# Kernel tuning notes

Measured on AMD Instinct MI355X. Metric: run time of the kernel, lower is better.

The kernel has to match this reference:

```python
import jax, jax.numpy as jnp
import numpy as np

T, N = 64, 128          # temporal / spatial graph sizes; M = T*N product-graph nodes
B, F_IN, HID, F_OUT = 2, 32, 32, 16
L, K = 2, 4             # num_layers, filter order


def _sym_norm(key, n):
    # random symmetric adjacency, then D^{-1/2} A D^{-1/2} / 2 as in the torch __init__
    a = jax.random.uniform(key, (n, n), dtype=jnp.float32)
    a = 0.5 * (a + a.T)
    d = jnp.sum(a, axis=1)
    dinv = 1.0 / jnp.sqrt(d)
    return (dinv[:, None] * a * dinv[None, :]) * 0.5


def setup_inputs() -> dict:
    key = jax.random.key(0)
    ks = jax.random.split(key, 9)
    x = jax.random.normal(ks[0], (B, T * N, F_IN), dtype=jnp.float32)
    Adj_t = _sym_norm(ks[1], T)
    Adj_s = _sym_norm(ks[2], N)
    s = jax.random.normal(ks[3], (4,), dtype=jnp.float32) * 0.25
    H = jax.random.normal(ks[4], (L, K, HID, HID), dtype=jnp.float32) * 0.1
    W1 = jax.random.normal(ks[5], (F_IN, HID), dtype=jnp.float32) * (1.0 / np.sqrt(F_IN))
    b1 = jax.random.normal(ks[6], (HID,), dtype=jnp.float32) * 0.01
    W2 = jax.random.normal(ks[7], (HID, F_OUT), dtype=jnp.float32) * (1.0 / np.sqrt(HID))
    b2 = jax.random.normal(ks[8], (F_OUT,), dtype=jnp.float32) * 0.01
    return {"x": x, "Adj_t": Adj_t, "Adj_s": Adj_s, "s": s, "H": H,
            "W1": W1, "b1": b1, "W2": W2, "b2": b2}


def reference(x, Adj_t, Adj_s, s, H, W1, b1, W2, b2):
    t, n = Adj_t.shape[0], Adj_s.shape[0]
    I_t = jnp.eye(t, dtype=jnp.float32)
    I_s = jnp.eye(n, dtype=jnp.float32)
    # Adj = s0*I + s1*kron(I_t, Adj_s) + s2*kron(Adj_t, I_s) + s3*kron(Adj_t, Adj_s)
    Adj = (s[0] * jnp.eye(t * n, dtype=jnp.float32)
           + s[1] * jnp.kron(I_t, Adj_s)
           + s[2] * jnp.kron(Adj_t, I_s)
           + s[3] * jnp.kron(Adj_t, Adj_s))
    h = x @ W1 + b1                                   # [B, M, HID]
    num_layers = H.shape[0]
    for l in range(num_layers):
        Ah = jnp.einsum('mn,bnh->bmh', Adj, h)        # Adj @ x, hoisted out of k-loop
        # sum_k (Adj@x) @ H[l,k]  ==  einsum over k and h simultaneously
        h = jnp.tanh(jnp.einsum('bmh,khf->bmf', Ah, H[l]))
    return h @ W2 + b2                                # [B, M, F_OUT]
```

## Files before the change

kernel.cpp:

```cpp
#include <hip/hip_runtime.h>


__device__ __forceinline__ int swz(int row, int g) { return g ^ (row & 7); }

template<bool PROJ>
__global__ __launch_bounds__(512) void k_temporal(
    const float* __restrict__ src,
    const float* __restrict__ At,
    const float* __restrict__ W1, const float* __restrict__ b1,
    const float* __restrict__ s,
    float* __restrict__ up, float* __restrict__ pp)
{
    __shared__ float At_s[64 * 64];
    __shared__ float xs  [64 * 32];
    __shared__ float hls [64 * 32];
    __shared__ float W1s [1024];

    const int tid = threadIdx.x;
    const int b   = blockIdx.x >> 7;
    const int n   = blockIdx.x & 127;
    const int fg  = tid >> 6;
    const int lt  = tid & 63;

    const float s0v = s[0], s1v = s[1], s2v = s[2], s3v = s[3];

#pragma unroll
    for (int i = 0; i < 8; ++i) {
        int p = tid + 512 * i;
        int r = p >> 6, c = p & 63;
        At_s[r * 64 + (swz(r, c >> 2) << 2) + (c & 3)] = At[p];
    }

    if (PROJ) {
        {
            int tt = tid >> 3, c4 = tid & 7;
            float4 v = *(const float4*)(src + ((size_t)(b * 8192 + tt * 128 + n)) * 32 + c4 * 4);
            *(float4*)&xs[tt * 32 + (swz(tt, c4) << 2)] = v;
        }
        if (tid < 256) ((float4*)W1s)[tid] = ((const float4*)W1)[tid];
        __syncthreads();
        float4 bv = *(const float4*)(b1 + fg * 4);
        float h0 = bv.x, h1 = bv.y, h2 = bv.z, h3 = bv.w;
#pragma unroll
        for (int k4 = 0; k4 < 8; ++k4) {
            float4 xv = *(const float4*)&xs[lt * 32 + (swz(lt, k4) << 2)];
            float4 w0 = *(const float4*)&W1s[(k4 * 4 + 0) * 32 + fg * 4];
            float4 w1 = *(const float4*)&W1s[(k4 * 4 + 1) * 32 + fg * 4];
            float4 w2 = *(const float4*)&W1s[(k4 * 4 + 2) * 32 + fg * 4];
            float4 w3 = *(const float4*)&W1s[(k4 * 4 + 3) * 32 + fg * 4];
            h0 += xv.x * w0.x + xv.y * w1.x + xv.z * w2.x + xv.w * w3.x;
            h1 += xv.x * w0.y + xv.y * w1.y + xv.z * w2.y + xv.w * w3.y;
            h2 += xv.x * w0.z + xv.y * w1.z + xv.z * w2.z + xv.w * w3.z;
            h3 += xv.x * w0.w + xv.y * w1.w + xv.z * w2.w + xv.w * w3.w;
        }
        float4 hv; hv.x = h0; hv.y = h1; hv.z = h2; hv.w = h3;
        *(float4*)&hls[lt * 32 + (swz(lt, fg) << 2)] = hv;
        __syncthreads();
    } else {
        {
            int tt = tid >> 3, c4 = tid & 7;
            float4 v = *(const float4*)(src + ((size_t)(b * 128 + n)) * 2048 + tt * 32 + c4 * 4);
            *(float4*)&hls[tt * 32 + (swz(tt, c4) << 2)] = v;
        }
        __syncthreads();
    }

    float4 hv = *(const float4*)&hls[lt * 32 + (swz(lt, fg) << 2)];
    float w0 = 0.f, w1 = 0.f, w2 = 0.f, w3 = 0.f;
#pragma unroll
    for (int u4 = 0; u4 < 16; ++u4) {
        float4 av = *(const float4*)&At_s[lt * 64 + (swz(lt, u4) << 2)];
        float4 g0 = *(const float4*)&hls[(u4 * 4 + 0) * 32 + (swz(u4 * 4 + 0, fg) << 2)];
        float4 g1 = *(const float4*)&hls[(u4 * 4 + 1) * 32 + (swz(u4 * 4 + 1, fg) << 2)];
        float4 g2 = *(const float4*)&hls[(u4 * 4 + 2) * 32 + (swz(u4 * 4 + 2, fg) << 2)];
        float4 g3 = *(const float4*)&hls[(u4 * 4 + 3) * 32 + (swz(u4 * 4 + 3, fg) << 2)];
        w0 += av.x * g0.x + av.y * g1.x + av.z * g2.x + av.w * g3.x;
        w1 += av.x * g0.y + av.y * g1.y + av.z * g2.y + av.w * g3.y;
        w2 += av.x * g0.z + av.y * g1.z + av.z * g2.z + av.w * g3.z;
        w3 += av.x * g0.w + av.y * g1.w + av.z * g2.w + av.w * g3.w;
    }
    float4 uo, po;
    uo.x = s1v * hv.x + s3v * w0;  po.x = s0v * hv.x + s2v * w0;
    uo.y = s1v * hv.y + s3v * w1;  po.y = s0v * hv.y + s2v * w1;
    uo.z = s1v * hv.z + s3v * w2;  po.z = s0v * hv.z + s2v * w2;
    uo.w = s1v * hv.w + s3v * w3;  po.w = s0v * hv.w + s2v * w3;
    size_t base = ((size_t)((b * 64 + lt) * 128 + n)) * 32 + fg * 4;
    *(float4*)(up + base) = uo;
    *(float4*)(pp + base) = po;
}

template<bool LAST>
__global__ __launch_bounds__(512) void k_spatial(
    const float* __restrict__ up, const float* __restrict__ pp,
    const float* __restrict__ As, const float* __restrict__ H, int layer,
    const float* __restrict__ W2, const float* __restrict__ b2,
    float* __restrict__ hout, float* __restrict__ out)
{
    __shared__ float As_s[64 * 128];
    __shared__ float up_s[128 * 32];
    __shared__ float Ah_s[64 * 32];
    __shared__ float T_s [64 * 32];
    __shared__ float Hs  [1024];
    __shared__ float W2s [512];

    const int tid = threadIdx.x;
    const int b   = blockIdx.x >> 7;
    const int t   = (blockIdx.x >> 1) & 63;
    const int mh  = blockIdx.x & 1;
    const int fg  = tid >> 6;
    const int m   = tid & 63;

#pragma unroll
    for (int i = 0; i < 4; ++i) {
        int p = tid + 512 * i;
        int r = p >> 5, g = p & 31;
        float4 v = *(const float4*)(As + ((size_t)(mh * 64 + r)) * 128 + g * 4);
        *(float4*)&As_s[r * 128 + (swz(r, g) << 2)] = v;
    }
    {
        const float* usrc = up + ((size_t)(b * 64 + t)) * 4096;
        ((float4*)up_s)[tid]       = ((const float4*)usrc)[tid];
        ((float4*)up_s)[tid + 512] = ((const float4*)usrc)[tid + 512];
    }
    {
        const float* Hl = H + layer * 4096;
#pragma unroll
        for (int i = 0; i < 2; ++i) {
            int p = tid + 512 * i;
            Hs[p] = Hl[p] + Hl[1024 + p] + Hl[2048 + p] + Hl[3072 + p];
        }
    }
    if (LAST && tid < 128) ((float4*)W2s)[tid] = ((const float4*)W2)[tid];
    float4 pv = *(const float4*)(pp + ((size_t)((b * 64 + t) * 128 + mh * 64 + m)) * 32 + fg * 4);
    float a0 = pv.x, a1 = pv.y, a2 = pv.z, a3 = pv.w;
    __syncthreads();

#pragma unroll 8
    for (int n4 = 0; n4 < 32; ++n4) {
        float4 av = *(const float4*)&As_s[m * 128 + (swz(m, n4) << 2)];
        float4 u0 = *(const float4*)&up_s[(n4 * 4 + 0) * 32 + fg * 4];
        float4 u1 = *(const float4*)&up_s[(n4 * 4 + 1) * 32 + fg * 4];
        float4 u2 = *(const float4*)&up_s[(n4 * 4 + 2) * 32 + fg * 4];
        float4 u3 = *(const float4*)&up_s[(n4 * 4 + 3) * 32 + fg * 4];
        a0 += av.x * u0.x + av.y * u1.x + av.z * u2.x + av.w * u3.x;
        a1 += av.x * u0.y + av.y * u1.y + av.z * u2.y + av.w * u3.y;
        a2 += av.x * u0.z + av.y * u1.z + av.z * u2.z + av.w * u3.z;
        a3 += av.x * u0.w + av.y * u1.w + av.z * u2.w + av.w * u3.w;
    }
    {
        float4 t4; t4.x = a0; t4.y = a1; t4.z = a2; t4.w = a3;
        *(float4*)&Ah_s[m * 32 + (swz(m, fg) << 2)] = t4;
    }
    __syncthreads();

    float c0 = 0.f, c1 = 0.f, c2 = 0.f, c3 = 0.f;
#pragma unroll
    for (int k4 = 0; k4 < 8; ++k4) {
        float4 av = *(const float4*)&Ah_s[m * 32 + (swz(m, k4) << 2)];
        float4 q0 = *(const float4*)&Hs[(k4 * 4 + 0) * 32 + fg * 4];
        float4 q1 = *(const float4*)&Hs[(k4 * 4 + 1) * 32 + fg * 4];
        float4 q2 = *(const float4*)&Hs[(k4 * 4 + 2) * 32 + fg * 4];
        float4 q3 = *(const float4*)&Hs[(k4 * 4 + 3) * 32 + fg * 4];
        c0 += av.x * q0.x + av.y * q1.x + av.z * q2.x + av.w * q3.x;
        c1 += av.x * q0.y + av.y * q1.y + av.z * q2.y + av.w * q3.y;
        c2 += av.x * q0.z + av.y * q1.z + av.z * q2.z + av.w * q3.z;
        c3 += av.x * q0.w + av.y * q1.w + av.z * q2.w + av.w * q3.w;
    }
    c0 = tanhf(c0); c1 = tanhf(c1); c2 = tanhf(c2); c3 = tanhf(c3);

    if (!LAST) {
        float4 o; o.x = c0; o.y = c1; o.z = c2; o.w = c3;
        *(float4*)(hout + (((size_t)(b * 128 + mh * 64 + m)) * 64 + t) * 32 + fg * 4) = o;
    } else {
        float4 t4; t4.x = c0; t4.y = c1; t4.z = c2; t4.w = c3;
        *(float4*)&T_s[m * 32 + (swz(m, fg) << 2)] = t4;
        __syncthreads();
        const int fo = fg * 2;
        float o0 = b2[fo], o1 = b2[fo + 1];
#pragma unroll
        for (int k4 = 0; k4 < 8; ++k4) {
            float4 tv = *(const float4*)&T_s[m * 32 + (swz(m, k4) << 2)];
            float2 v0 = *(const float2*)&W2s[(k4 * 4 + 0) * 16 + fo];
            float2 v1 = *(const float2*)&W2s[(k4 * 4 + 1) * 16 + fo];
            float2 v2 = *(const float2*)&W2s[(k4 * 4 + 2) * 16 + fo];
            float2 v3 = *(const float2*)&W2s[(k4 * 4 + 3) * 16 + fo];
            o0 += tv.x * v0.x + tv.y * v1.x + tv.z * v2.x + tv.w * v3.x;
            o1 += tv.x * v0.y + tv.y * v1.y + tv.z * v2.y + tv.w * v3.y;
        }
        float2 o2; o2.x = o0; o2.y = o1;
        *(float2*)(out + ((size_t)((b * 64 + t) * 128 + mh * 64 + m)) * 16 + fo) = o2;
    }
}

extern "C" void kernel_launch(void* const* d_in, const int* in_sizes, int n_in,
                              void* d_out, int out_size, void* d_ws, size_t ws_size,
                              hipStream_t stream)
{
    const float* x   = (const float*)d_in[0];
    const float* At  = (const float*)d_in[1];
    const float* As  = (const float*)d_in[2];
    const float* s   = (const float*)d_in[3];
    const float* H   = (const float*)d_in[4];
    const float* W1  = (const float*)d_in[5];
    const float* b1  = (const float*)d_in[6];
    const float* W2  = (const float*)d_in[7];
    const float* b2  = (const float*)d_in[8];
    float* out = (float*)d_out;

    float* up   = (float*)d_ws;
    float* pp   = up + 524288;
    float* hbuf = pp + 524288;

    k_temporal<true ><<<256, 512, 0, stream>>>(x,    At, W1, b1, s, up, pp);
    k_spatial <false><<<256, 512, 0, stream>>>(up, pp, As, H, 0, W2, b2, hbuf, out);
    k_temporal<false><<<256, 512, 0, stream>>>(hbuf, At, W1, b1, s, up, pp);
    k_spatial <true ><<<256, 512, 0, stream>>>(up, pp, As, H, 1, W2, b2, hbuf, out);
}
```

Baseline: 32.77 us.

## Broadcast matrix operands via wave readlane instead of shared-memory staging

Weight matrices (W1, summed H, W2) and intermediate activations (h, up rows) are kept distributed in registers across the 64 lanes of a wave. Their per-element values are broadcast with readlane into SGPRs, replacing the float4 LDS loads and the shared buffers that staged them. This removes LDS traffic and shared-memory footprint, which can help occupancy, and drops some barriers. The cost is many scalar readlane instructions, each serialized per wave, plus a fully unrolled spatial loop that raises code size and register pressure.

Result: slower. 34.20 us (+4.4%).

```diff
diff --git a/kernel.cpp b/kernel.cpp
--- a/kernel.cpp
+++ b/kernel.cpp
@@ -2,6 +2,10 @@
 
 
 __device__ __forceinline__ int swz(int row, int g) { return g ^ (row & 7); }
+
+__device__ __forceinline__ float rlane(float v, int lane) {
+    return __builtin_bit_cast(float, __builtin_amdgcn_readlane(__builtin_bit_cast(int, v), lane));
+}
 
 template<bool PROJ>
 __global__ __launch_bounds__(512) void k_temporal(
@@ -13,8 +17,6 @@
 {
     __shared__ float At_s[64 * 64];
     __shared__ float xs  [64 * 32];
-    __shared__ float hls [64 * 32];
-    __shared__ float W1s [1024];
 
     const int tid = threadIdx.x;
     const int b   = blockIdx.x >> 7;
@@ -31,59 +33,55 @@
         At_s[r * 64 + (swz(r, c >> 2) << 2) + (c & 3)] = At[p];
     }
 
+    float h0, h1, h2, h3;
     if (PROJ) {
         {
             int tt = tid >> 3, c4 = tid & 7;
             float4 v = *(const float4*)(src + ((size_t)(b * 8192 + tt * 128 + n)) * 32 + c4 * 4);
             *(float4*)&xs[tt * 32 + (swz(tt, c4) << 2)] = v;
         }
-        if (tid < 256) ((float4*)W1s)[tid] = ((const float4*)W1)[tid];
+        float4 w1r = *(const float4*)(W1 + (lt & 31) * 32 + fg * 4);
+        float4 bv  = *(const float4*)(b1 + fg * 4);
         __syncthreads();
-        float4 bv = *(const float4*)(b1 + fg * 4);
-        float h0 = bv.x, h1 = bv.y, h2 = bv.z, h3 = bv.w;
+        h0 = bv.x; h1 = bv.y; h2 = bv.z; h3 = bv.w;
 #pragma unroll
         for (int k4 = 0; k4 < 8; ++k4) {
             float4 xv = *(const float4*)&xs[lt * 32 + (swz(lt, k4) << 2)];
-            float4 w0 = *(const float4*)&W1s[(k4 * 4 + 0) * 32 + fg * 4];
-            float4 w1 = *(const float4*)&W1s[(k4 * 4 + 1) * 32 + fg * 4];
-            float4 w2 = *(const float4*)&W1s[(k4 * 4 + 2) * 32 + fg * 4];
-            float4 w3 = *(const float4*)&W1s[(k4 * 4 + 3) * 32 + fg * 4];
-            h0 += xv.x * w0.x + xv.y * w1.x + xv.z * w2.x + xv.w * w3.x;
-            h1 += xv.x * w0.y + xv.y * w1.y + xv.z * w2.y + xv.w * w3.y;
-            h2 += xv.x * w0.z + xv.y * w1.z + xv.z * w2.z + xv.w * w3.z;
-            h3 += xv.x * w0.w + xv.y * w1.w + xv.z * w2.w + xv.w * w3.w;
+#define PROJSTEP(a, k)                                   \
+            h0 += (a) * rlane(w1r.x, (k));               \
+            h1 += (a) * rlane(w1r.y, (k));               \
+            h2 += (a) * rlane(w1r.z, (k));               \
+            h3 += (a) * rlane(w1r.w, (k));
+            PROJSTEP(xv.x, k4 * 4 + 0)
+            PROJSTEP(xv.y, k4 * 4 + 1)
+            PROJSTEP(xv.z, k4 * 4 + 2)
+            PROJSTEP(xv.w, k4 * 4 + 3)
         }
-        float4 hv; hv.x = h0; hv.y = h1; hv.z = h2; hv.w = h3;
-        *(float4*)&hls[lt * 32 + (swz(lt, fg) << 2)] = hv;
+    } else {
+        float4 hv = *(const float4*)(src + (((size_t)(b * 128 + n)) * 64 + lt) * 32 + fg * 4);
+        h0 = hv.x; h1 = hv.y; h2 = hv.z; h3 = hv.w;
         __syncthreads();
-    } else {
-        {
-            int tt = tid >> 3, c4 = tid & 7;
-            float4 v = *(const float4*)(src + ((size_t)(b * 128 + n)) * 2048 + tt * 32 + c4 * 4);
-            *(float4*)&hls[tt * 32 + (swz(tt, c4) << 2)] = v;
-        }
-        __syncthreads();
-    }
-
-    float4 hv = *(const float4*)&hls[lt * 32 + (swz(lt, fg) << 2)];
+    }
+
     float w0 = 0.f, w1 = 0.f, w2 = 0.f, w3 = 0.f;
 #pragma unroll
     for (int u4 = 0; u4 < 16; ++u4) {
         float4 av = *(const float4*)&At_s[lt * 64 + (swz(lt, u4) << 2)];
-        float4 g0 = *(const float4*)&hls[(u4 * 4 + 0) * 32 + (swz(u4 * 4 + 0, fg) << 2)];
-        float4 g1 = *(const float4*)&hls[(u4 * 4 + 1) * 32 + (swz(u4 * 4 + 1, fg) << 2)];
-        float4 g2 = *(const float4*)&hls[(u4 * 4 + 2) * 32 + (swz(u4 * 4 + 2, fg) << 2)];
-        float4 g3 = *(const float4*)&hls[(u4 * 4 + 3) * 32 + (swz(u4 * 4 + 3, fg) << 2)];
-        w0 += av.x * g0.x + av.y * g1.x + av.z * g2.x + av.w * g3.x;
-        w1 += av.x * g0.y + av.y * g1.y + av.z * g2.y + av.w * g3.y;
-        w2 += av.x * g0.z + av.y * g1.z + av.z * g2.z + av.w * g3.z;
-        w3 += av.x * g0.w + av.y * g1.w + av.z * g2.w + av.w * g3.w;
+#define MIXSTEP(a, u)                                    \
+        w0 += (a) * rlane(h0, (u));                      \
+        w1 += (a) * rlane(h1, (u));                      \
+        w2 += (a) * rlane(h2, (u));                      \
+        w3 += (a) * rlane(h3, (u));
+        MIXSTEP(av.x, u4 * 4 + 0)
+        MIXSTEP(av.y, u4 * 4 + 1)
+        MIXSTEP(av.z, u4 * 4 + 2)
+        MIXSTEP(av.w, u4 * 4 + 3)
     }
     float4 uo, po;
-    uo.x = s1v * hv.x + s3v * w0;  po.x = s0v * hv.x + s2v * w0;
-    uo.y = s1v * hv.y + s3v * w1;  po.y = s0v * hv.y + s2v * w1;
-    uo.z = s1v * hv.z + s3v * w2;  po.z = s0v * hv.z + s2v * w2;
-    uo.w = s1v * hv.w + s3v * w3;  po.w = s0v * hv.w + s2v * w3;
+    uo.x = s1v * h0 + s3v * w0;  po.x = s0v * h0 + s2v * w0;
+    uo.y = s1v * h1 + s3v * w1;  po.y = s0v * h1 + s2v * w1;
+    uo.z = s1v * h2 + s3v * w2;  po.z = s0v * h2 + s2v * w2;
+    uo.w = s1v * h3 + s3v * w3;  po.w = s0v * h3 + s2v * w3;
     size_t base = ((size_t)((b * 64 + lt) * 128 + n)) * 32 + fg * 4;
     *(float4*)(up + base) = uo;
     *(float4*)(pp + base) = po;
@@ -97,11 +95,8 @@
     float* __restrict__ hout, float* __restrict__ out)
 {
     __shared__ float As_s[64 * 128];
-    __shared__ float up_s[128 * 32];
     __shared__ float Ah_s[64 * 32];
     __shared__ float T_s [64 * 32];
-    __shared__ float Hs  [1024];
-    __shared__ float W2s [512];
 
     const int tid = threadIdx.x;
     const int b   = blockIdx.x >> 7;
@@ -117,35 +112,42 @@
         float4 v = *(const float4*)(As + ((size_t)(mh * 64 + r)) * 128 + g * 4);
         *(float4*)&As_s[r * 128 + (swz(r, g) << 2)] = v;
     }
+    const float* urow = up + ((size_t)(b * 64 + t)) * 4096;
+    float4 ua = *(const float4*)(urow + (2 * m)     * 32 + fg * 4);
+    float4 ub = *(const float4*)(urow + (2 * m + 1) * 32 + fg * 4);
+    float4 hsr;
     {
-        const float* usrc = up + ((size_t)(b * 64 + t)) * 4096;
-        ((float4*)up_s)[tid]       = ((const float4*)usrc)[tid];
-        ((float4*)up_s)[tid + 512] = ((const float4*)usrc)[tid + 512];
-    }
-    {
-        const float* Hl = H + layer * 4096;
-#pragma unroll
-        for (int i = 0; i < 2; ++i) {
-            int p = tid + 512 * i;
-            Hs[p] = Hl[p] + Hl[1024 + p] + Hl[2048 + p] + Hl[3072 + p];
-        }
-    }
-    if (LAST && tid < 128) ((float4*)W2s)[tid] = ((const float4*)W2)[tid];
+        const float* Hl = H + layer * 4096 + (m & 31) * 32 + fg * 4;
+        float4 q0 = *(const float4*)(Hl);
+        float4 q1 = *(const float4*)(Hl + 1024);
+        float4 q2 = *(const float4*)(Hl + 2048);
+        float4 q3 = *(const float4*)(Hl + 3072);
+        hsr.x = q0.x + q1.x + q2.x + q3.x;
+        hsr.y = q0.y + q1.y + q2.y + q3.y;
+        hsr.z = q0.z + q1.z + q2.z + q3.z;
+        hsr.w = q0.w + q1.w + q2.w + q3.w;
+    }
+    float2 w2r, b2v;
+    if (LAST) {
+        w2r = *(const float2*)(W2 + (m & 31) * 16 + fg * 2);
+        b2v = *(const float2*)(b2 + fg * 2);
+    }
     float4 pv = *(const float4*)(pp + ((size_t)((b * 64 + t) * 128 + mh * 64 + m)) * 32 + fg * 4);
     float a0 = pv.x, a1 = pv.y, a2 = pv.z, a3 = pv.w;
     __syncthreads();
 
-#pragma unroll 8
+#pragma unroll
     for (int n4 = 0; n4 < 32; ++n4) {
         float4 av = *(const float4*)&As_s[m * 128 + (swz(m, n4) << 2)];
-        float4 u0 = *(const float4*)&up_s[(n4 * 4 + 0) * 32 + fg * 4];
-        float4 u1 = *(const float4*)&up_s[(n4 * 4 + 1) * 32 + fg * 4];
-        float4 u2 = *(const float4*)&up_s[(n4 * 4 + 2) * 32 + fg * 4];
-        float4 u3 = *(const float4*)&up_s[(n4 * 4 + 3) * 32 + fg * 4];
-        a0 += av.x * u0.x + av.y * u1.x + av.z * u2.x + av.w * u3.x;
-        a1 += av.x * u0.y + av.y * u1.y + av.z * u2.y + av.w * u3.y;
-        a2 += av.x * u0.z + av.y * u1.z + av.z * u2.z + av.w * u3.z;
-        a3 += av.x * u0.w + av.y * u1.w + av.z * u2.w + av.w * u3.w;
+#define SPSTEP(a, reg, ln)                               \
+        a0 += (a) * rlane(reg.x, (ln));                  \
+        a1 += (a) * rlane(reg.y, (ln));                  \
+        a2 += (a) * rlane(reg.z, (ln));                  \
+        a3 += (a) * rlane(reg.w, (ln));
+        SPSTEP(av.x, ua, 2 * n4)
+        SPSTEP(av.y, ub, 2 * n4)
+        SPSTEP(av.z, ua, 2 * n4 + 1)
+        SPSTEP(av.w, ub, 2 * n4 + 1)
     }
     {
         float4 t4; t4.x = a0; t4.y = a1; t4.z = a2; t4.w = a3;
@@ -157,14 +159,15 @@
 #pragma unroll
     for (int k4 = 0; k4 < 8; ++k4) {
         float4 av = *(const float4*)&Ah_s[m * 32 + (swz(m, k4) << 2)];
-        float4 q0 = *(const float4*)&Hs[(k4 * 4 + 0) * 32 + fg * 4];
-        float4 q1 = *(const float4*)&Hs[(k4 * 4 + 1) * 32 + fg * 4];
-        float4 q2 = *(const float4*)&Hs[(k4 * 4 + 2) * 32 + fg * 4];
-        float4 q3 = *(const float4*)&Hs[(k4 * 4 + 3) * 32 + fg * 4];
-        c0 += av.x * q0.x + av.y * q1.x + av.z * q2.x + av.w * q3.x;
-        c1 += av.x * q0.y + av.y * q1.y + av.z * q2.y + av.w * q3.y;
-        c2 += av.x * q0.z + av.y * q1.z + av.z * q2.z + av.w * q3.z;
-        c3 += av.x * q0.w + av.y * q1.w + av.z * q2.w + av.w * q3.w;
+#define FSTEP(a, k)                                      \
+        c0 += (a) * rlane(hsr.x, (k));                   \
+        c1 += (a) * rlane(hsr.y, (k));                   \
+        c2 += (a) * rlane(hsr.z, (k));                   \
+        c3 += (a) * rlane(hsr.w, (k));
+        FSTEP(av.x, k4 * 4 + 0)
+        FSTEP(av.y, k4 * 4 + 1)
+        FSTEP(av.z, k4 * 4 + 2)
+        FSTEP(av.w, k4 * 4 + 3)
     }
     c0 = tanhf(c0); c1 = tanhf(c1); c2 = tanhf(c2); c3 = tanhf(c3);
 
@@ -175,20 +178,20 @@
         float4 t4; t4.x = c0; t4.y = c1; t4.z = c2; t4.w = c3;
         *(float4*)&T_s[m * 32 + (swz(m, fg) << 2)] = t4;
         __syncthreads();
-        const int fo = fg * 2;
-        float o0 = b2[fo], o1 = b2[fo + 1];
+        float o0 = b2v.x, o1 = b2v.y;
 #pragma unroll
         for (int k4 = 0; k4 < 8; ++k4) {
             float4 tv = *(const float4*)&T_s[m * 32 + (swz(m, k4) << 2)];
-            float2 v0 = *(const float2*)&W2s[(k4 * 4 + 0) * 16 + fo];
-            float2 v1 = *(const float2*)&W2s[(k4 * 4 + 1) * 16 + fo];
-            float2 v2 = *(const float2*)&W2s[(k4 * 4 + 2) * 16 + fo];
-            float2 v3 = *(const float2*)&W2s[(k4 * 4 + 3) * 16 + fo];
-            o0 += tv.x * v0.x + tv.y * v1.x + tv.z * v2.x + tv.w * v3.x;
-            o1 += tv.x * v0.y + tv.y * v1.y + tv.z * v2.y + tv.w * v3.y;
+#define OSTEP(a, k)                                      \
+            o0 += (a) * rlane(w2r.x, (k));               \
+            o1 += (a) * rlane(w2r.y, (k));
+            OSTEP(tv.x, k4 * 4 + 0)
+            OSTEP(tv.y, k4 * 4 + 1)
+            OSTEP(tv.z, k4 * 4 + 2)
+            OSTEP(tv.w, k4 * 4 + 3)
         }
         float2 o2; o2.x = o0; o2.y = o1;
-        *(float2*)(out + ((size_t)((b * 64 + t) * 128 + mh * 64 + m)) * 16 + fo) = o2;
+        *(float2*)(out + ((size_t)((b * 64 + t) * 128 + mh * 64 + m)) * 16 + fg * 2) = o2;
     }
 }
 
```
